# Optimization experiments

Measured on AMD Instinct MI355X. Metric: run time of the kernel, lower is better.

## Reference

```python
import jax, jax.numpy as jnp
import numpy as np

EMB = 4096
NUM_EXPERTS = 64
TOP_K = 2
TOKENS = 16384


def setup_inputs() -> dict:
    key = jax.random.key(0)
    kx, kw, kb = jax.random.split(key, 3)
    x = jax.random.normal(kx, (TOKENS, EMB), dtype=jnp.float32)
    # nn.Linear(emb_size, num_experts): weight [num_experts, emb], bias [num_experts]
    W = jax.random.normal(kw, (NUM_EXPERTS, EMB), dtype=jnp.float32) / np.sqrt(EMB)
    b = jax.random.normal(kb, (NUM_EXPERTS,), dtype=jnp.float32) * 0.01
    return {"x": x, "W": W, "b": b}


def reference(x, W, b):
    # logits = x @ W.T + b  -> [tokens, num_experts]
    logits = jnp.einsum("td,ed->te", x, W) + b
    topk_val, topk_idx = jax.lax.top_k(logits, TOP_K)  # [tokens, k]
    probs = jax.nn.softmax(topk_val, axis=-1)
    return (topk_idx, probs)
```

## Files before the change

### kernel.cpp

```cpp
#include <hip/hip_runtime.h>

#define TOKENS 16384
#define EMB 4096
#define NEXP 64
#define BK 64

typedef __attribute__((ext_vector_type(8))) short short8;
typedef __attribute__((ext_vector_type(4))) float f32x4;
typedef __attribute__((ext_vector_type(4))) unsigned short ush4;

#define WP_USHORTS (3 * NEXP * EMB)
#define WP_FLOATS  (WP_USHORTS / 2)

__device__ __forceinline__ void gl_lds16(const void* g, void* lds) {
    __builtin_amdgcn_global_load_lds(
        (const __attribute__((address_space(1))) void*)g,
        (__attribute__((address_space(3))) void*)lds, 16, 0, 0);
}

__device__ __forceinline__ void split3(float x, unsigned short& h,
                                       unsigned short& m, unsigned short& l) {
    unsigned u = __float_as_uint(x);
    unsigned r = u + 0x7FFFu + ((u >> 16) & 1u);
    float hF = __uint_as_float(r & 0xFFFF0000u);
    h = (unsigned short)(r >> 16);
    float r1 = x - hF;
    unsigned u1 = __float_as_uint(r1);
    float mF = __uint_as_float(u1 & 0xFFFF0000u);
    m = (unsigned short)(u1 >> 16);
    float r2 = r1 - mF;
    l = (unsigned short)(__float_as_uint(r2) >> 16);
}

__device__ __forceinline__ void split3_pair(float x0, float x1,
        unsigned& hw, unsigned& mw, unsigned& lw) {
    unsigned u0 = __float_as_uint(x0), u1 = __float_as_uint(x1);
    unsigned r0 = u0 + 0x7FFFu + ((u0 >> 16) & 1u);
    unsigned r1 = u1 + 0x7FFFu + ((u1 >> 16) & 1u);
    hw = __builtin_amdgcn_perm(r1, r0, 0x07060302u);
    float s0 = x0 - __uint_as_float(r0 & 0xFFFF0000u);
    float s1 = x1 - __uint_as_float(r1 & 0xFFFF0000u);
    unsigned v0 = __float_as_uint(s0), v1 = __float_as_uint(s1);
    mw = __builtin_amdgcn_perm(v1, v0, 0x07060302u);
    float t0 = s0 - __uint_as_float(v0 & 0xFFFF0000u);
    float t1 = s1 - __uint_as_float(v1 & 0xFFFF0000u);
    lw = __builtin_amdgcn_perm(__float_as_uint(t1), __float_as_uint(t0), 0x07060302u);
}

__device__ __forceinline__ void build_frags(const float4& a0, const float4& a1,
        short8& H, short8& M, short8& L) {
    union { short8 v; unsigned u[4]; } h_, m_, l_;
    split3_pair(a0.x, a0.y, h_.u[0], m_.u[0], l_.u[0]);
    split3_pair(a0.z, a0.w, h_.u[1], m_.u[1], l_.u[1]);
    split3_pair(a1.x, a1.y, h_.u[2], m_.u[2], l_.u[2]);
    split3_pair(a1.z, a1.w, h_.u[3], m_.u[3], l_.u[3]);
    H = h_.v; M = m_.v; L = l_.v;
}

__global__ __launch_bounds__(256) void split_w(const float* __restrict__ W,
                                               unsigned short* __restrict__ Wp) {
    const int i = (blockIdx.x * 256 + threadIdx.x) * 4;
    const float4 v = *reinterpret_cast<const float4*>(W + i);
    ush4 h, m, l;
#pragma unroll
    for (int e = 0; e < 4; ++e) {
        unsigned short he, me, le;
        split3(reinterpret_cast<const float*>(&v)[e], he, me, le);
        h[e] = he; m[e] = me; l[e] = le;
    }
    *reinterpret_cast<ush4*>(Wp + i) = h;
    *reinterpret_cast<ush4*>(Wp + NEXP * EMB + i) = m;
    *reinterpret_cast<ush4*>(Wp + 2 * NEXP * EMB + i) = l;
}

template<int S>
__global__ __launch_bounds__(256, 2) void router_mfma(
    const float* __restrict__ x, const unsigned short* __restrict__ Wp,
    float* __restrict__ part)
{
    constexpr int KPER = EMB / S;
    constexpr int NCH  = KPER / BK;

    __shared__ unsigned short sB[3][192][BK];

    const int t  = threadIdx.x;
    const int w  = t >> 6;
    const int l  = t & 63;
    const int lr = l & 15;
    const int lo = l >> 4;
    const int tok0 = blockIdx.x * 128 + w * 32;
    const int kb   = blockIdx.y * KPER;

    const float* ax[2];
    ax[0] = x + (size_t)(tok0 + lr) * EMB + kb + lo * 8;
    ax[1] = x + (size_t)(tok0 + 16 + lr) * EMB + kb + lo * 8;

    const unsigned short* gb[6];
#pragma unroll
    for (int p = 0; p < 6; ++p)
        gb[p] = Wp + (size_t)(48 * w + 8 * p + (l >> 3)) * EMB + kb
              + 8 * ((l & 7) ^ ((l >> 3) & 7));

    f32x4 accH[2][4], accL[2][4];
#pragma unroll
    for (int ti = 0; ti < 2; ++ti)
#pragma unroll
        for (int et = 0; et < 4; ++et) {
            accH[ti][et] = (f32x4){0.f, 0.f, 0.f, 0.f};
            accL[ti][et] = (f32x4){0.f, 0.f, 0.f, 0.f};
        }

    float4 ac[2][2][2], an[2][2][2];
#pragma unroll
    for (int p = 0; p < 6; ++p)
        gl_lds16(gb[p], &sB[0][48 * w + 8 * p][0]);
#pragma unroll
    for (int ti = 0; ti < 2; ++ti)
#pragma unroll
        for (int h = 0; h < 2; ++h) {
            ac[ti][h][0] = *reinterpret_cast<const float4*>(ax[ti] + 32 * h);
            ac[ti][h][1] = *reinterpret_cast<const float4*>(ax[ti] + 32 * h + 4);
        }
#pragma unroll
    for (int p = 0; p < 6; ++p)
        gl_lds16(gb[p] + BK, &sB[1][48 * w + 8 * p][0]);

    int buf = 0;
#pragma unroll 1
    for (int ks = 0; ks < NCH; ++ks) {
        asm volatile("s_waitcnt vmcnt(6)" ::: "memory");
        __builtin_amdgcn_s_barrier();

        if (ks + 1 < NCH) {
#pragma unroll
            for (int ti = 0; ti < 2; ++ti)
#pragma unroll
                for (int h = 0; h < 2; ++h) {
                    an[ti][h][0] = *reinterpret_cast<const float4*>(
                        ax[ti] + (ks + 1) * BK + 32 * h);
                    an[ti][h][1] = *reinterpret_cast<const float4*>(
                        ax[ti] + (ks + 1) * BK + 32 * h + 4);
                }
        }
        if (ks + 2 < NCH) {
            const int sb = (buf == 0) ? 2 : buf - 1;
#pragma unroll
            for (int p = 0; p < 6; ++p)
                gl_lds16(gb[p] + (ks + 2) * BK, &sB[sb][48 * w + 8 * p][0]);
        }
        __builtin_amdgcn_sched_barrier(0);

#pragma unroll
        for (int h = 0; h < 2; ++h) {
            short8 aH0, aM0, aL0, aH1, aM1, aL1;
            build_frags(ac[0][h][0], ac[0][h][1], aH0, aM0, aL0);
            build_frags(ac[1][h][0], ac[1][h][1], aH1, aM1, aL1);
            const int sw = ((4 * h + lo) ^ (lr & 7)) * 8;
#pragma unroll
            for (int et = 0; et < 4; ++et) {
                const unsigned short* bp = &sB[buf][et * 16 + lr][sw];
                const short8 bH = *reinterpret_cast<const short8*>(bp);
                const short8 bM = *reinterpret_cast<const short8*>(bp + 64 * BK);
                const short8 bL = *reinterpret_cast<const short8*>(bp + 128 * BK);
                accH[0][et] = __builtin_amdgcn_mfma_f32_16x16x32_bf16(aH0, bH, accH[0][et], 0, 0, 0);
                accL[0][et] = __builtin_amdgcn_mfma_f32_16x16x32_bf16(aH0, bM, accL[0][et], 0, 0, 0);
                accL[0][et] = __builtin_amdgcn_mfma_f32_16x16x32_bf16(aM0, bH, accL[0][et], 0, 0, 0);
                accL[0][et] = __builtin_amdgcn_mfma_f32_16x16x32_bf16(aM0, bM, accL[0][et], 0, 0, 0);
                accL[0][et] = __builtin_amdgcn_mfma_f32_16x16x32_bf16(aH0, bL, accL[0][et], 0, 0, 0);
                accL[0][et] = __builtin_amdgcn_mfma_f32_16x16x32_bf16(aL0, bH, accL[0][et], 0, 0, 0);
                accH[1][et] = __builtin_amdgcn_mfma_f32_16x16x32_bf16(aH1, bH, accH[1][et], 0, 0, 0);
                accL[1][et] = __builtin_amdgcn_mfma_f32_16x16x32_bf16(aH1, bM, accL[1][et], 0, 0, 0);
                accL[1][et] = __builtin_amdgcn_mfma_f32_16x16x32_bf16(aM1, bH, accL[1][et], 0, 0, 0);
                accL[1][et] = __builtin_amdgcn_mfma_f32_16x16x32_bf16(aM1, bM, accL[1][et], 0, 0, 0);
                accL[1][et] = __builtin_amdgcn_mfma_f32_16x16x32_bf16(aH1, bL, accL[1][et], 0, 0, 0);
                accL[1][et] = __builtin_amdgcn_mfma_f32_16x16x32_bf16(aL1, bH, accL[1][et], 0, 0, 0);
            }
        }
#pragma unroll
        for (int ti = 0; ti < 2; ++ti)
#pragma unroll
            for (int h = 0; h < 2; ++h) {
                ac[ti][h][0] = an[ti][h][0];
                ac[ti][h][1] = an[ti][h][1];
            }
        buf = (buf == 2) ? 0 : buf + 1;
    }

    __syncthreads();
    float* sled = reinterpret_cast<float*>(&sB[0][0][0]) + w * 2112;
#pragma unroll
    for (int ti = 0; ti < 2; ++ti)
#pragma unroll
        for (int et = 0; et < 4; ++et)
#pragma unroll
            for (int j = 0; j < 4; ++j)
                sled[(et * 16 + lr) * 33 + ti * 16 + lo * 4 + j]
                    = accH[ti][et][j] + accL[ti][et][j];
#pragma unroll
    for (int r = 0; r < 32; ++r) {
        const int e = 2 * r + (l >> 5);
        part[(size_t)(blockIdx.y * NEXP + e) * TOKENS + tok0 + (l & 31)]
            = sled[e * 33 + (l & 31)];
    }
}

template<int S>
__global__ __launch_bounds__(256) void reduce_topk(
    const float* __restrict__ part, const float* __restrict__ b,
    float* __restrict__ out)
{
    __shared__ double sv[64][4][2];
    __shared__ int    si[64][4][2];
    const int t    = threadIdx.x;
    const int p4   = t & 3;
    const int slot = t >> 2;
    const int tok  = blockIdx.x * 64 + slot;

    double v[16];
#pragma unroll
    for (int j = 0; j < 16; ++j) v[j] = 0.0;
    for (int s = 0; s < S; ++s)
#pragma unroll
        for (int j = 0; j < 16; ++j)
            v[j] += (double)part[(size_t)((s << 6) + (p4 << 4) + j) * TOKENS + tok];
#pragma unroll
    for (int j = 0; j < 16; ++j) v[j] += (double)b[(p4 << 4) + j];

    double v1 = -1e300, v2 = -1e300; int i1 = 0, i2 = 0;
#pragma unroll
    for (int j = 0; j < 16; ++j) {
        const int e = (p4 << 4) + j;
        if (v[j] > v1)      { v2 = v1; i2 = i1; v1 = v[j]; i1 = e; }
        else if (v[j] > v2) { v2 = v[j]; i2 = e; }
    }
    sv[slot][p4][0] = v1; sv[slot][p4][1] = v2;
    si[slot][p4][0] = i1; si[slot][p4][1] = i2;
    __syncthreads();

    if (p4 == 0) {
        double m1 = -1e300, m2 = -1e300; int j1 = 0, j2 = 0;
#pragma unroll
        for (int p = 0; p < 4; ++p)
#pragma unroll
            for (int r = 0; r < 2; ++r) {
                const double vv = sv[slot][p][r]; const int ii = si[slot][p][r];
                if (vv > m1)      { m2 = m1; j2 = j1; m1 = vv; j1 = ii; }
                else if (vv > m2) { m2 = vv; j2 = ii; }
            }
        const float e2  = expf((float)(m2 - m1));
        const float inv = 1.0f / (1.0f + e2);
        out[2 * tok]     = (float)j1;
        out[2 * tok + 1] = (float)j2;
        out[2 * TOKENS + 2 * tok]     = inv;
        out[2 * TOKENS + 2 * tok + 1] = e2 * inv;
    }
}

extern "C" void kernel_launch(void* const* d_in, const int* in_sizes, int n_in,
                              void* d_out, int out_size, void* d_ws, size_t ws_size,
                              hipStream_t stream) {
    const float* x = (const float*)d_in[0];
    const float* W = (const float*)d_in[1];
    const float* b = (const float*)d_in[2];
    float* out = (float*)d_out;
    unsigned short* Wp = (unsigned short*)d_ws;
    float* part = (float*)d_ws + WP_FLOATS;

    split_w<<<dim3(NEXP * EMB / 1024), dim3(256), 0, stream>>>(W, Wp);

    const size_t base = (size_t)WP_FLOATS * 4;
    const size_t per  = (size_t)NEXP * TOKENS * 4;
    if (ws_size >= base + 4 * per) {
        router_mfma<4><<<dim3(TOKENS / 128, 4), dim3(256), 0, stream>>>(x, Wp, part);
        reduce_topk<4><<<dim3(TOKENS / 64), dim3(256), 0, stream>>>(part, b, out);
    } else if (ws_size >= base + 2 * per) {
        router_mfma<2><<<dim3(TOKENS / 128, 2), dim3(256), 0, stream>>>(x, Wp, part);
        reduce_topk<2><<<dim3(TOKENS / 64), dim3(256), 0, stream>>>(part, b, out);
    } else {
        router_mfma<1><<<dim3(TOKENS / 128, 1), dim3(256), 0, stream>>>(x, Wp, part);
        reduce_topk<1><<<dim3(TOKENS / 64), dim3(256), 0, stream>>>(part, b, out);
    }
}
```

Before: 81.12 us.

## Restructure router GEMM pipeline with smaller K tiles, double buffering, 8-way split-K

Halves the K chunk to 32 and switches the W tiles from triple to double LDS buffering, with a manually unrolled two-stage loop that ping-pongs register A fragments. The smaller LDS footprint lets occupancy rise to 3 blocks per CU, and a new 8-way split-K path adds more parallel blocks. Partial sums are now written in token-major layout straight from registers, skipping the LDS transpose, and the reduce kernel reads them with float4 loads. The risks are more partial-sum traffic to reduce and the loss of the LDS swizzle, which may cause bank conflicts. The S=1 fallback is also removed, so a small workspace now takes the S=2 path.

```diff
diff --git a/kernel.cpp b/kernel.cpp
--- a/kernel.cpp
+++ b/kernel.cpp
@@ -3,7 +3,7 @@
 #define TOKENS 16384
 #define EMB 4096
 #define NEXP 64
-#define BK 64
+#define BK 32
 
 typedef __attribute__((ext_vector_type(8))) short short8;
 typedef __attribute__((ext_vector_type(4))) float f32x4;
@@ -73,15 +73,54 @@
     *reinterpret_cast<ush4*>(Wp + 2 * NEXP * EMB + i) = l;
 }
 
+#define MFMA_BLOCK(BUFC, AH0, AM0, AL0, AH1, AM1, AL1)                          \
+    _Pragma("unroll")                                                           \
+    for (int et = 0; et < 4; ++et) {                                            \
+        const unsigned short* bp = &sB[BUFC][et * 16 + lr][lo * 8];             \
+        const short8 bH = *reinterpret_cast<const short8*>(bp);                 \
+        const short8 bM = *reinterpret_cast<const short8*>(bp + 64 * BK);       \
+        const short8 bL = *reinterpret_cast<const short8*>(bp + 128 * BK);      \
+        accH[0][et] = __builtin_amdgcn_mfma_f32_16x16x32_bf16(AH0, bH, accH[0][et], 0, 0, 0); \
+        accL[0][et] = __builtin_amdgcn_mfma_f32_16x16x32_bf16(AH0, bM, accL[0][et], 0, 0, 0); \
+        accL[0][et] = __builtin_amdgcn_mfma_f32_16x16x32_bf16(AM0, bH, accL[0][et], 0, 0, 0); \
+        accL[0][et] = __builtin_amdgcn_mfma_f32_16x16x32_bf16(AM0, bM, accL[0][et], 0, 0, 0); \
+        accL[0][et] = __builtin_amdgcn_mfma_f32_16x16x32_bf16(AH0, bL, accL[0][et], 0, 0, 0); \
+        accL[0][et] = __builtin_amdgcn_mfma_f32_16x16x32_bf16(AL0, bH, accL[0][et], 0, 0, 0); \
+        accH[1][et] = __builtin_amdgcn_mfma_f32_16x16x32_bf16(AH1, bH, accH[1][et], 0, 0, 0); \
+        accL[1][et] = __builtin_amdgcn_mfma_f32_16x16x32_bf16(AH1, bM, accL[1][et], 0, 0, 0); \
+        accL[1][et] = __builtin_amdgcn_mfma_f32_16x16x32_bf16(AM1, bH, accL[1][et], 0, 0, 0); \
+        accL[1][et] = __builtin_amdgcn_mfma_f32_16x16x32_bf16(AM1, bM, accL[1][et], 0, 0, 0); \
+        accL[1][et] = __builtin_amdgcn_mfma_f32_16x16x32_bf16(AH1, bL, accL[1][et], 0, 0, 0); \
+        accL[1][et] = __builtin_amdgcn_mfma_f32_16x16x32_bf16(AL1, bH, accL[1][et], 0, 0, 0); \
+    }
+
+#define BODY_MAIN(KS, AC, BUFC) do {                                            \
+    asm volatile("s_waitcnt vmcnt(4)" ::: "memory");                            \
+    __builtin_amdgcn_s_barrier();                                               \
+    _Pragma("unroll")                                                           \
+    for (int p = 0; p < 3; ++p)                                                 \
+        gl_lds16(gb[p] + ((KS) + 1) * BK, &sB[(BUFC) ^ 1][48 * w + 16 * p][0]); \
+    short8 aH0, aM0, aL0, aH1, aM1, aL1;                                        \
+    build_frags(AC[0][0], AC[0][1], aH0, aM0, aL0);                             \
+    build_frags(AC[1][0], AC[1][1], aH1, aM1, aL1);                             \
+    _Pragma("unroll")                                                           \
+    for (int ti = 0; ti < 2; ++ti) {                                            \
+        AC[ti][0] = *reinterpret_cast<const float4*>(ax[ti] + ((KS) + 2) * BK);     \
+        AC[ti][1] = *reinterpret_cast<const float4*>(ax[ti] + ((KS) + 2) * BK + 4); \
+    }                                                                           \
+    __builtin_amdgcn_sched_barrier(0);                                          \
+    MFMA_BLOCK(BUFC, aH0, aM0, aL0, aH1, aM1, aL1)                              \
+} while (0)
+
 template<int S>
-__global__ __launch_bounds__(256, 2) void router_mfma(
+__global__ __launch_bounds__(256, 3) void router_mfma(
     const float* __restrict__ x, const unsigned short* __restrict__ Wp,
     float* __restrict__ part)
 {
     constexpr int KPER = EMB / S;
     constexpr int NCH  = KPER / BK;
 
-    __shared__ unsigned short sB[3][192][BK];
+    __shared__ unsigned short sB[2][192][BK];
 
     const int t  = threadIdx.x;
     const int w  = t >> 6;
@@ -95,11 +134,10 @@
     ax[0] = x + (size_t)(tok0 + lr) * EMB + kb + lo * 8;
     ax[1] = x + (size_t)(tok0 + 16 + lr) * EMB + kb + lo * 8;
 
-    const unsigned short* gb[6];
-#pragma unroll
-    for (int p = 0; p < 6; ++p)
-        gb[p] = Wp + (size_t)(48 * w + 8 * p + (l >> 3)) * EMB + kb
-              + 8 * ((l & 7) ^ ((l >> 3) & 7));
+    const unsigned short* gb[3];
+#pragma unroll
+    for (int p = 0; p < 3; ++p)
+        gb[p] = Wp + (size_t)(48 * w + 16 * p + (l >> 2)) * EMB + kb + 8 * (l & 3);
 
     f32x4 accH[2][4], accL[2][4];
 #pragma unroll
@@ -110,98 +148,57 @@
             accL[ti][et] = (f32x4){0.f, 0.f, 0.f, 0.f};
         }
 
-    float4 ac[2][2][2], an[2][2][2];
-#pragma unroll
-    for (int p = 0; p < 6; ++p)
-        gl_lds16(gb[p], &sB[0][48 * w + 8 * p][0]);
+    float4 aA[2][2], aB[2][2];
+#pragma unroll
+    for (int ti = 0; ti < 2; ++ti) {
+        aA[ti][0] = *reinterpret_cast<const float4*>(ax[ti]);
+        aA[ti][1] = *reinterpret_cast<const float4*>(ax[ti] + 4);
+    }
+#pragma unroll
+    for (int p = 0; p < 3; ++p)
+        gl_lds16(gb[p], &sB[0][48 * w + 16 * p][0]);
+#pragma unroll
+    for (int ti = 0; ti < 2; ++ti) {
+        aB[ti][0] = *reinterpret_cast<const float4*>(ax[ti] + BK);
+        aB[ti][1] = *reinterpret_cast<const float4*>(ax[ti] + BK + 4);
+    }
+
+#pragma unroll 1
+    for (int kt = 0; kt < NCH - 2; kt += 2) {
+        BODY_MAIN(kt, aA, 0);
+        BODY_MAIN(kt + 1, aB, 1);
+    }
+
+    {
+        asm volatile("s_waitcnt vmcnt(4)" ::: "memory");
+        __builtin_amdgcn_s_barrier();
+#pragma unroll
+        for (int p = 0; p < 3; ++p)
+            gl_lds16(gb[p] + (NCH - 1) * BK, &sB[1][48 * w + 16 * p][0]);
+        short8 aH0, aM0, aL0, aH1, aM1, aL1;
+        build_frags(aA[0][0], aA[0][1], aH0, aM0, aL0);
+        build_frags(aA[1][0], aA[1][1], aH1, aM1, aL1);
+        MFMA_BLOCK(0, aH0, aM0, aL0, aH1, aM1, aL1)
+    }
+    {
+        asm volatile("s_waitcnt vmcnt(0)" ::: "memory");
+        __builtin_amdgcn_s_barrier();
+        short8 aH0, aM0, aL0, aH1, aM1, aL1;
+        build_frags(aB[0][0], aB[0][1], aH0, aM0, aL0);
+        build_frags(aB[1][0], aB[1][1], aH1, aM1, aL1);
+        MFMA_BLOCK(1, aH0, aM0, aL0, aH1, aM1, aL1)
+    }
+
 #pragma unroll
     for (int ti = 0; ti < 2; ++ti)
 #pragma unroll
-        for (int h = 0; h < 2; ++h) {
-            ac[ti][h][0] = *reinterpret_cast<const float4*>(ax[ti] + 32 * h);
-            ac[ti][h][1] = *reinterpret_cast<const float4*>(ax[ti] + 32 * h + 4);
-        }
-#pragma unroll
-    for (int p = 0; p < 6; ++p)
-        gl_lds16(gb[p] + BK, &sB[1][48 * w + 8 * p][0]);
-
-    int buf = 0;
-#pragma unroll 1
-    for (int ks = 0; ks < NCH; ++ks) {
-        asm volatile("s_waitcnt vmcnt(6)" ::: "memory");
-        __builtin_amdgcn_s_barrier();
-
-        if (ks + 1 < NCH) {
-#pragma unroll
-            for (int ti = 0; ti < 2; ++ti)
-#pragma unroll
-                for (int h = 0; h < 2; ++h) {
-                    an[ti][h][0] = *reinterpret_cast<const float4*>(
-                        ax[ti] + (ks + 1) * BK + 32 * h);
-                    an[ti][h][1] = *reinterpret_cast<const float4*>(
-                        ax[ti] + (ks + 1) * BK + 32 * h + 4);
-                }
-        }
-        if (ks + 2 < NCH) {
-            const int sb = (buf == 0) ? 2 : buf - 1;
-#pragma unroll
-            for (int p = 0; p < 6; ++p)
-                gl_lds16(gb[p] + (ks + 2) * BK, &sB[sb][48 * w + 8 * p][0]);
-        }
-        __builtin_amdgcn_sched_barrier(0);
-
-#pragma unroll
-        for (int h = 0; h < 2; ++h) {
-            short8 aH0, aM0, aL0, aH1, aM1, aL1;
-            build_frags(ac[0][h][0], ac[0][h][1], aH0, aM0, aL0);
-            build_frags(ac[1][h][0], ac[1][h][1], aH1, aM1, aL1);
-            const int sw = ((4 * h + lo) ^ (lr & 7)) * 8;
-#pragma unroll
-            for (int et = 0; et < 4; ++et) {
-                const unsigned short* bp = &sB[buf][et * 16 + lr][sw];
-                const short8 bH = *reinterpret_cast<const short8*>(bp);
-                const short8 bM = *reinterpret_cast<const short8*>(bp + 64 * BK);
-                const short8 bL = *reinterpret_cast<const short8*>(bp + 128 * BK);
-                accH[0][et] = __builtin_amdgcn_mfma_f32_16x16x32_bf16(aH0, bH, accH[0][et], 0, 0, 0);
-                accL[0][et] = __builtin_amdgcn_mfma_f32_16x16x32_bf16(aH0, bM, accL[0][et], 0, 0, 0);
-                accL[0][et] = __builtin_amdgcn_mfma_f32_16x16x32_bf16(aM0, bH, accL[0][et], 0, 0, 0);
-                accL[0][et] = __builtin_amdgcn_mfma_f32_16x16x32_bf16(aM0, bM, accL[0][et], 0, 0, 0);
-                accL[0][et] = __builtin_amdgcn_mfma_f32_16x16x32_bf16(aH0, bL, accL[0][et], 0, 0, 0);
-                accL[0][et] = __builtin_amdgcn_mfma_f32_16x16x32_bf16(aL0, bH, accL[0][et], 0, 0, 0);
-                accH[1][et] = __builtin_amdgcn_mfma_f32_16x16x32_bf16(aH1, bH, accH[1][et], 0, 0, 0);
-                accL[1][et] = __builtin_amdgcn_mfma_f32_16x16x32_bf16(aH1, bM, accL[1][et], 0, 0, 0);
-                accL[1][et] = __builtin_amdgcn_mfma_f32_16x16x32_bf16(aM1, bH, accL[1][et], 0, 0, 0);
-                accL[1][et] = __builtin_amdgcn_mfma_f32_16x16x32_bf16(aM1, bM, accL[1][et], 0, 0, 0);
-                accL[1][et] = __builtin_amdgcn_mfma_f32_16x16x32_bf16(aH1, bL, accL[1][et], 0, 0, 0);
-                accL[1][et] = __builtin_amdgcn_mfma_f32_16x16x32_bf16(aL1, bH, accL[1][et], 0, 0, 0);
+        for (int et = 0; et < 4; ++et)
+#pragma unroll
+            for (int j = 0; j < 4; ++j) {
+                const int tok = tok0 + ti * 16 + lo * 4 + j;
+                part[((size_t)blockIdx.y * TOKENS + tok) * NEXP + et * 16 + lr]
+                    = accH[ti][et][j] + accL[ti][et][j];
             }
-        }
-#pragma unroll
-        for (int ti = 0; ti < 2; ++ti)
-#pragma unroll
-            for (int h = 0; h < 2; ++h) {
-                ac[ti][h][0] = an[ti][h][0];
-                ac[ti][h][1] = an[ti][h][1];
-            }
-        buf = (buf == 2) ? 0 : buf + 1;
-    }
-
-    __syncthreads();
-    float* sled = reinterpret_cast<float*>(&sB[0][0][0]) + w * 2112;
-#pragma unroll
-    for (int ti = 0; ti < 2; ++ti)
-#pragma unroll
-        for (int et = 0; et < 4; ++et)
-#pragma unroll
-            for (int j = 0; j < 4; ++j)
-                sled[(et * 16 + lr) * 33 + ti * 16 + lo * 4 + j]
-                    = accH[ti][et][j] + accL[ti][et][j];
-#pragma unroll
-    for (int r = 0; r < 32; ++r) {
-        const int e = 2 * r + (l >> 5);
-        part[(size_t)(blockIdx.y * NEXP + e) * TOKENS + tok0 + (l & 31)]
-            = sled[e * 33 + (l & 31)];
-    }
 }
 
 template<int S>
@@ -219,10 +216,18 @@
     double v[16];
 #pragma unroll
     for (int j = 0; j < 16; ++j) v[j] = 0.0;
-    for (int s = 0; s < S; ++s)
-#pragma unroll
-        for (int j = 0; j < 16; ++j)
-            v[j] += (double)part[(size_t)((s << 6) + (p4 << 4) + j) * TOKENS + tok];
+    for (int s = 0; s < S; ++s) {
+        const float4* pp = reinterpret_cast<const float4*>(
+            part + ((size_t)s * TOKENS + tok) * NEXP + (p4 << 4));
+#pragma unroll
+        for (int q = 0; q < 4; ++q) {
+            const float4 f = pp[q];
+            v[4 * q + 0] += (double)f.x;
+            v[4 * q + 1] += (double)f.y;
+            v[4 * q + 2] += (double)f.z;
+            v[4 * q + 3] += (double)f.w;
+        }
+    }
 #pragma unroll
     for (int j = 0; j < 16; ++j) v[j] += (double)b[(p4 << 4) + j];
 
@@ -269,15 +274,15 @@
     split_w<<<dim3(NEXP * EMB / 1024), dim3(256), 0, stream>>>(W, Wp);
 
     const size_t base = (size_t)WP_FLOATS * 4;
-    const size_t per  = (size_t)NEXP * TOKENS * 4;
-    if (ws_size >= base + 4 * per) {
+    const size_t per  = (size_t)TOKENS * NEXP * 4;
+    if (ws_size >= base + 8 * per) {
+        router_mfma<8><<<dim3(TOKENS / 128, 8), dim3(256), 0, stream>>>(x, Wp, part);
+        reduce_topk<8><<<dim3(TOKENS / 64), dim3(256), 0, stream>>>(part, b, out);
+    } else if (ws_size >= base + 4 * per) {
         router_mfma<4><<<dim3(TOKENS / 128, 4), dim3(256), 0, stream>>>(x, Wp, part);
         reduce_topk<4><<<dim3(TOKENS / 64), dim3(256), 0, stream>>>(part, b, out);
-    } else if (ws_size >= base + 2 * per) {
+    } else {
         router_mfma<2><<<dim3(TOKENS / 128, 2), dim3(256), 0, stream>>>(x, Wp, part);
         reduce_topk<2><<<dim3(TOKENS / 64), dim3(256), 0, stream>>>(part, b, out);
-    } else {
-        router_mfma<1><<<dim3(TOKENS / 128, 1), dim3(256), 0, stream>>>(x, Wp, part);
-        reduce_topk<1><<<dim3(TOKENS / 64), dim3(256), 0, stream>>>(part, b, out);
-    }
-}
+    }
+}
```

Measured after the change: 85.04 us. +4.8%, slower.
